# Optimization experiments

Measured on AMD Instinct MI355X. Metric: run time of the kernel, lower is better.

Reference implementation:

```python
import jax, jax.numpy as jnp
import numpy as np

B, S, D = 2, 2048, 1024
E, K, F = 8, 2, 4 * D


def setup_inputs() -> dict:
    key = jax.random.key(0)
    ks = jax.random.split(key, 5)
    sd = 1.0 / np.sqrt(D)
    sf = 1.0 / np.sqrt(F)
    x = jax.random.normal(ks[0], (B, S, D), dtype=jnp.float32)
    Wg = jax.random.uniform(ks[1], (D, E), dtype=jnp.float32, minval=-sd, maxval=sd)
    W1 = jax.random.uniform(ks[2], (E, D, F), dtype=jnp.float32, minval=-sd, maxval=sd)
    W3 = jax.random.uniform(ks[3], (D, E * F), dtype=jnp.float32, minval=-sd, maxval=sd).reshape(D, E, F).transpose(1, 0, 2)
    W2 = jax.random.uniform(ks[4], (E, F, D), dtype=jnp.float32, minval=-sf, maxval=sf)
    return {"x": x, "Wg": Wg, "W1": W1, "W2": W2, "W3": W3}


def reference(x, Wg, W1, W2, W3):
    Bx, Sx, Dx = x.shape
    xf = x.reshape(-1, Dx)  # [T, D]
    T = xf.shape[0]
    gate_logits = xf @ Wg  # [T, E]
    probs = jax.nn.softmax(gate_logits, axis=-1)
    weights, sel = jax.lax.top_k(probs, K)  # [T, K]
    weights = weights / jnp.sum(weights, axis=-1, keepdims=True)
    # scatter top-k weights into a dense [T, E] combine matrix (top-k indices are distinct)
    coef = jnp.zeros((T, W1.shape[0]), dtype=xf.dtype)
    coef = coef.at[jnp.arange(T)[:, None], sel].add(weights)
    out = jnp.zeros_like(xf)
    for e in range(W1.shape[0]):  # small fixed expert count
        h = jax.nn.silu(xf @ W1[e]) * (xf @ W3[e])  # [T, F]
        out = out + coef[:, e:e + 1] * (h @ W2[e])
    aux_loss = jnp.mean(jnp.var(gate_logits, axis=-1, ddof=1))  # torch .var() is unbiased
    return out.reshape(Bx, Sx, Dx), aux_loss
```

## Files before the change

kernel.cpp:

```cpp
#include <hip/hip_runtime.h>

typedef __bf16 bf16x8 __attribute__((ext_vector_type(8)));
typedef float  f32x4  __attribute__((ext_vector_type(4)));

#define TOKS 4096
#define DIM  1024
#define NEXP 8
#define NF   4096
#define CAP  4096
#define BM 128
#define BN 128
#define BK 64

typedef __attribute__((address_space(3))) unsigned int as3_u32;
typedef __attribute__((address_space(1))) unsigned int as1_u32;
__device__ __forceinline__ void gl16(const unsigned short* g, unsigned short* l) {
  __builtin_amdgcn_global_load_lds((as1_u32*)(unsigned long long)g, (as3_u32*)l, 16, 0, 0);
}

__device__ __forceinline__ unsigned short f2bf(float f) {
  unsigned int u = __float_as_uint(f);
  u += 0x7FFFu + ((u >> 16) & 1u);
  return (unsigned short)(u >> 16);
}
__device__ __forceinline__ int swzo(int major) {
  return ((major & 7) ^ ((major >> 3) & 7)) << 3;
}
__device__ __forceinline__ int swz8(int row, int chunk) {
  return (chunk ^ (row & 7)) << 3;
}

__global__ void moe_route(const float* __restrict__ x, const float* __restrict__ Wg,
                          int* __restrict__ pairCnt, int* __restrict__ pairIdx,
                          float* __restrict__ pairWgt, float* __restrict__ auxSum)
{
  int lane = threadIdx.x & 63;
  int tok  = blockIdx.x * 4 + (threadIdx.x >> 6);
  const float* xr = x + (size_t)tok * DIM;
  float acc[8];
  #pragma unroll
  for (int e = 0; e < 8; ++e) acc[e] = 0.f;
  #pragma unroll
  for (int i = 0; i < 16; ++i) {
    int d = i * 64 + lane;
    float xv = xr[d];
    const float4* wr = (const float4*)(Wg + d * 8);
    float4 wa = wr[0], wb = wr[1];
    acc[0] += xv * wa.x; acc[1] += xv * wa.y; acc[2] += xv * wa.z; acc[3] += xv * wa.w;
    acc[4] += xv * wb.x; acc[5] += xv * wb.y; acc[6] += xv * wb.z; acc[7] += xv * wb.w;
  }
  #pragma unroll
  for (int e = 0; e < 8; ++e) {
    float v = acc[e];
    #pragma unroll
    for (int off = 32; off; off >>= 1) v += __shfl_xor(v, off);
    acc[e] = v;
  }
  if (lane == 0) {
    int e1 = 0; float l1 = acc[0];
    #pragma unroll
    for (int e = 1; e < 8; ++e) if (acc[e] > l1) { l1 = acc[e]; e1 = e; }
    int e2 = -1; float l2 = -3.4e38f;
    #pragma unroll
    for (int e = 0; e < 8; ++e) if (e != e1 && acc[e] > l2) { l2 = acc[e]; e2 = e; }
    float r  = expf(l2 - l1);
    float w1 = 1.f / (1.f + r);
    float w2 = r / (1.f + r);
    int s1 = atomicAdd(&pairCnt[e1], 1);
    pairIdx[e1 * CAP + s1] = tok * 2;     pairWgt[e1 * CAP + s1] = w1;
    int s2 = atomicAdd(&pairCnt[e2], 1);
    pairIdx[e2 * CAP + s2] = tok * 2 + 1; pairWgt[e2 * CAP + s2] = w2;
    float m = 0.f;
    #pragma unroll
    for (int e = 0; e < 8; ++e) m += acc[e];
    m *= 0.125f;
    float v = 0.f;
    #pragma unroll
    for (int e = 0; e < 8; ++e) { float dd = acc[e] - m; v += dd * dd; }
    atomicAdd(auxSum, v * (1.f / 7.f));
  }
}

__global__ void moe_aux_final(const float* __restrict__ auxSum, float* __restrict__ outScalar) {
  *outScalar = auxSum[0] * (1.f / (float)TOKS);
}

__global__ __launch_bounds__(256) void cvt_x(const float* __restrict__ in,
                                             unsigned short* __restrict__ o)
{
  int i = (blockIdx.x * 256 + threadIdx.x) * 16;
  const float4* s = (const float4*)(in + i);
  float4 a = s[0], b = s[1], c = s[2], d = s[3];
  union { unsigned short u[8]; uint4 q; } p0, p1;
  p0.u[0]=f2bf(a.x); p0.u[1]=f2bf(a.y); p0.u[2]=f2bf(a.z); p0.u[3]=f2bf(a.w);
  p0.u[4]=f2bf(b.x); p0.u[5]=f2bf(b.y); p0.u[6]=f2bf(b.z); p0.u[7]=f2bf(b.w);
  p1.u[0]=f2bf(c.x); p1.u[1]=f2bf(c.y); p1.u[2]=f2bf(c.z); p1.u[3]=f2bf(c.w);
  p1.u[4]=f2bf(d.x); p1.u[5]=f2bf(d.y); p1.u[6]=f2bf(d.z); p1.u[7]=f2bf(d.w);
  *(uint4*)(o + i)     = p0.q;
  *(uint4*)(o + i + 8) = p1.q;
}

__global__ __launch_bounds__(256) void cvt_transpose(
    const float* __restrict__ in, unsigned short* __restrict__ outp, int R, int C)
{
  __shared__ unsigned short tile[64 * 72];
  int e  = blockIdx.z;
  int r0 = blockIdx.x * 64, c0 = blockIdx.y * 64;
  const float*    ine  = in   + (size_t)e * R * C;
  unsigned short* oute = outp + (size_t)e * R * C;
  int t = threadIdx.x;
  int r = t >> 2, cs = (t & 3) * 16;
  const float4* src = (const float4*)(ine + (size_t)(r0 + r) * C + c0 + cs);
  #pragma unroll
  for (int j = 0; j < 4; ++j) {
    float4 v = src[j];
    tile[(cs + j * 4 + 0) * 72 + r] = f2bf(v.x);
    tile[(cs + j * 4 + 1) * 72 + r] = f2bf(v.y);
    tile[(cs + j * 4 + 2) * 72 + r] = f2bf(v.z);
    tile[(cs + j * 4 + 3) * 72 + r] = f2bf(v.w);
  }
  __syncthreads();
  int c = t >> 2, rs = (t & 3) * 16;
  uint4 o0 = *(const uint4*)&tile[c * 72 + rs];
  uint4 o1 = *(const uint4*)&tile[c * 72 + rs + 8];
  unsigned short* dst = oute + (size_t)(c0 + c) * R + r0 + rs;
  *(uint4*)dst       = o0;
  *(uint4*)(dst + 8) = o1;
}

__global__ __launch_bounds__(256) void cvt_w13(
    const float* __restrict__ W1, const float* __restrict__ W3,
    unsigned short* __restrict__ outp)
{
  __shared__ unsigned short t1[64 * 72];
  __shared__ unsigned short t3[64 * 72];
  int e  = blockIdx.z;
  int r0 = blockIdx.x * 64, c0 = blockIdx.y * 64;
  const float* in1 = W1 + (size_t)e * DIM * NF;
  const float* in3 = W3 + (size_t)e * DIM * NF;
  unsigned short* oute = outp + (size_t)e * (2 * NF) * DIM;
  int t = threadIdx.x;
  int r = t >> 2, cs = (t & 3) * 16;
  const float4* s1 = (const float4*)(in1 + (size_t)(r0 + r) * NF + c0 + cs);
  const float4* s3 = (const float4*)(in3 + (size_t)(r0 + r) * NF + c0 + cs);
  #pragma unroll
  for (int j = 0; j < 4; ++j) {
    float4 v1 = s1[j];
    float4 v3 = s3[j];
    int cb = cs + j * 4;
    t1[(cb + 0) * 72 + r] = f2bf(v1.x);
    t1[(cb + 1) * 72 + r] = f2bf(v1.y);
    t1[(cb + 2) * 72 + r] = f2bf(v1.z);
    t1[(cb + 3) * 72 + r] = f2bf(v1.w);
    t3[(cb + 0) * 72 + r] = f2bf(v3.x);
    t3[(cb + 1) * 72 + r] = f2bf(v3.y);
    t3[(cb + 2) * 72 + r] = f2bf(v3.z);
    t3[(cb + 3) * 72 + r] = f2bf(v3.w);
  }
  __syncthreads();
  int c = t >> 2, rs = (t & 3) * 16;
  int drow = c0 * 2 + (c >> 4) * 32 + (c & 15);
  uint4 a0 = *(const uint4*)&t1[c * 72 + rs];
  uint4 a1 = *(const uint4*)&t1[c * 72 + rs + 8];
  uint4 b0 = *(const uint4*)&t3[c * 72 + rs];
  uint4 b1 = *(const uint4*)&t3[c * 72 + rs + 8];
  unsigned short* d1 = oute + (size_t)drow * DIM + r0 + rs;
  unsigned short* d3 = d1 + (size_t)16 * DIM;
  *(uint4*)d1       = a0;
  *(uint4*)(d1 + 8) = a1;
  *(uint4*)d3       = b0;
  *(uint4*)(d3 + 8) = b1;
}

__global__ __launch_bounds__(512) void moe_ffn1_i(
    const unsigned short* __restrict__ xbf, const unsigned short* __restrict__ W13T,
    const int* __restrict__ pairCnt, const int* __restrict__ pairIdx,
    unsigned short* __restrict__ hbuf)
{
  int bid = blockIdx.x;
  int m_t = (bid >> 3) & 31;
  int n_t = (bid & 7) | (((bid >> 8) & 7) << 3);
  int e   = bid >> 11;
  int cnt = pairCnt[e];
  int m0  = m_t * BM;
  if (m0 >= cnt) return;
  int n0f = n_t * 64;
  __shared__ __attribute__((aligned(16))) unsigned short As[BM * BK];
  __shared__ __attribute__((aligned(16))) unsigned short Bs[BN * BK];
  __shared__ int rowPid[BM];
  int tid = threadIdx.x, lane = tid & 63, wid = tid >> 6;
  if (tid < BM) {
    int gi = m0 + tid;
    rowPid[tid] = (gi < cnt) ? pairIdx[e * CAP + gi] : -1;
  }
  const unsigned short* W13e = W13T + (size_t)e * (2 * NF) * DIM + (size_t)n_t * 128 * DIM;
  f32x4 zero = {0.f, 0.f, 0.f, 0.f};
  f32x4 acc[2][4];
  #pragma unroll
  for (int mi = 0; mi < 2; ++mi)
    #pragma unroll
    for (int ni = 0; ni < 4; ++ni) acc[mi][ni] = zero;
  int wm = (wid >> 1) * 32, wn = (wid & 1) * 64;
  __syncthreads();

  int r0a = wid * 16 + (lane >> 3), r1a = r0a + 8;
  int p0 = rowPid[r0a], p1 = rowPid[r1a];
  size_t tk0 = (size_t)((p0 >= 0) ? (p0 >> 1) : 0);
  size_t tk1 = (size_t)((p1 >= 0) ? (p1 >> 1) : 0);
  int ch0 = ((lane & 7) ^ (r0a & 7)) * 8;
  int ch1 = ((lane & 7) ^ (r1a & 7)) * 8;
  const unsigned short* gA0 = xbf + tk0 * DIM + ch0;
  const unsigned short* gA1 = xbf + tk1 * DIM + ch1;
  const unsigned short* gB0 = W13e + (size_t)r0a * DIM + ch0;
  const unsigned short* gB1 = W13e + (size_t)r1a * DIM + ch1;
  unsigned short* lA0 = &As[(wid * 16) * BK];
  unsigned short* lA1 = &As[(wid * 16 + 8) * BK];
  unsigned short* lB0 = &Bs[(wid * 16) * BK];
  unsigned short* lB1 = &Bs[(wid * 16 + 8) * BK];

  for (int kt = 0; kt < DIM; kt += BK) {
    gl16(gA0 + kt, lA0); gl16(gA1 + kt, lA1);
    gl16(gB0 + kt, lB0); gl16(gB1 + kt, lB1);
    __syncthreads();
    #pragma unroll
    for (int ks = 0; ks < 2; ++ks) {
      int kc = ks * 4 + (lane >> 4);
      bf16x8 af[2];
      #pragma unroll
      for (int mi = 0; mi < 2; ++mi) {
        int row = wm + mi * 16 + (lane & 15);
        af[mi] = *(const bf16x8*)(&As[row * BK + swz8(row, kc)]);
      }
      #pragma unroll
      for (int ni = 0; ni < 4; ++ni) {
        int br = wn + ni * 16 + (lane & 15);
        bf16x8 b = *(const bf16x8*)(&Bs[br * BK + swz8(br, kc)]);
        #pragma unroll
        for (int mi = 0; mi < 2; ++mi)
          acc[mi][ni] = __builtin_amdgcn_mfma_f32_16x16x32_bf16(af[mi], b, acc[mi][ni], 0, 0, 0);
      }
    }
    __syncthreads();
  }
  #pragma unroll
  for (int mi = 0; mi < 2; ++mi) {
    #pragma unroll
    for (int r = 0; r < 4; ++r) {
      int row = wm + mi * 16 + ((lane >> 4) << 2) + r;
      int pid = rowPid[row];
      if (pid < 0) continue;
      size_t hb = (size_t)pid * NF + n0f + (wn >> 1) + (lane & 15);
      #pragma unroll
      for (int fg = 0; fg < 2; ++fg) {
        float a = acc[mi][fg * 2 + 0][r];
        float g = acc[mi][fg * 2 + 1][r];
        float s = 1.f / (1.f + __expf(-a));
        hbuf[hb + fg * 16] = f2bf(a * s * g);
      }
    }
  }
}

__global__ __launch_bounds__(512) void moe_ffn2_g(
    const unsigned short* __restrict__ hbuf, const unsigned short* __restrict__ W2T,
    const int* __restrict__ pairCnt, const int* __restrict__ pairIdx,
    const float* __restrict__ pairWgt, float* __restrict__ out)
{
  int bid = blockIdx.x;
  int n_t = bid & 7;
  int m_t = (bid >> 3) & 31;
  int e   = bid >> 8;
  int cnt = pairCnt[e];
  int m0  = m_t * BM;
  if (m0 >= cnt) return;
  int n0  = n_t * BN;
  __shared__ __attribute__((aligned(16))) unsigned short As[BM * BK];
  __shared__ __attribute__((aligned(16))) unsigned short Bs[BN * BK];
  __shared__ int   rowPid[BM];
  __shared__ float rowW[BM];
  int tid = threadIdx.x, lane = tid & 63, wid = tid >> 6;
  if (tid < BM) {
    int gi = m0 + tid;
    if (gi < cnt) { rowPid[tid] = pairIdx[e * CAP + gi]; rowW[tid] = pairWgt[e * CAP + gi]; }
    else          { rowPid[tid] = -1;                    rowW[tid] = 0.f; }
  }
  const unsigned short* W2e = W2T + (size_t)e * DIM * NF + (size_t)n0 * NF;
  f32x4 zero = {0.f, 0.f, 0.f, 0.f};
  f32x4 acc[2][4];
  #pragma unroll
  for (int mi = 0; mi < 2; ++mi)
    #pragma unroll
    for (int ni = 0; ni < 4; ++ni) acc[mi][ni] = zero;
  int wm = (wid >> 1) * 32, wn = (wid & 1) * 64;
  __syncthreads();

  int r0a = wid * 16 + (lane >> 3), r1a = r0a + 8;
  int p0 = rowPid[r0a], p1 = rowPid[r1a];
  size_t h0 = (size_t)((p0 >= 0) ? p0 : 0);
  size_t h1 = (size_t)((p1 >= 0) ? p1 : 0);
  int ch0 = ((lane & 7) ^ (r0a & 7)) * 8;
  int ch1 = ((lane & 7) ^ (r1a & 7)) * 8;
  const unsigned short* gA0 = hbuf + h0 * NF + ch0;
  const unsigned short* gA1 = hbuf + h1 * NF + ch1;
  const unsigned short* gB0 = W2e + (size_t)r0a * NF + ch0;
  const unsigned short* gB1 = W2e + (size_t)r1a * NF + ch1;
  unsigned short* lA0 = &As[(wid * 16) * BK];
  unsigned short* lA1 = &As[(wid * 16 + 8) * BK];
  unsigned short* lB0 = &Bs[(wid * 16) * BK];
  unsigned short* lB1 = &Bs[(wid * 16 + 8) * BK];

  for (int kt = 0; kt < NF; kt += BK) {
    gl16(gA0 + kt, lA0); gl16(gA1 + kt, lA1);
    gl16(gB0 + kt, lB0); gl16(gB1 + kt, lB1);
    __syncthreads();
    #pragma unroll
    for (int ks = 0; ks < 2; ++ks) {
      int kc = ks * 4 + (lane >> 4);
      bf16x8 af[2];
      #pragma unroll
      for (int mi = 0; mi < 2; ++mi) {
        int row = wm + mi * 16 + (lane & 15);
        af[mi] = *(const bf16x8*)(&As[row * BK + swz8(row, kc)]);
      }
      #pragma unroll
      for (int ni = 0; ni < 4; ++ni) {
        int dc = wn + ni * 16 + (lane & 15);
        bf16x8 b = *(const bf16x8*)(&Bs[dc * BK + swz8(dc, kc)]);
        #pragma unroll
        for (int mi = 0; mi < 2; ++mi)
          acc[mi][ni] = __builtin_amdgcn_mfma_f32_16x16x32_bf16(af[mi], b, acc[mi][ni], 0, 0, 0);
      }
    }
    __syncthreads();
  }
  #pragma unroll
  for (int mi = 0; mi < 2; ++mi) {
    #pragma unroll
    for (int r = 0; r < 4; ++r) {
      int row = wm + mi * 16 + ((lane >> 4) << 2) + r;
      int pid = rowPid[row];
      if (pid < 0) continue;
      float w = rowW[row];
      float* op = out + (size_t)(pid >> 1) * DIM + n0 + wn + (lane & 15);
      #pragma unroll
      for (int ni = 0; ni < 4; ++ni)
        atomicAdd(op + ni * 16, w * acc[mi][ni][r]);
    }
  }
}

__global__ __launch_bounds__(512) void moe_ffn1(
    const float* __restrict__ x, const float* __restrict__ W1, const float* __restrict__ W3,
    const int* __restrict__ pairCnt, const int* __restrict__ pairIdx,
    unsigned short* __restrict__ hbuf)
{
  int e   = blockIdx.z;
  int cnt = pairCnt[e];
  int m0  = blockIdx.x * BM;
  if (m0 >= cnt) return;
  int n0  = blockIdx.y * BN;
  __shared__ __attribute__((aligned(16))) unsigned short As[BM * BK];
  __shared__ __attribute__((aligned(16))) unsigned short B1s[BN * BK];
  __shared__ __attribute__((aligned(16))) unsigned short B3s[BN * BK];
  __shared__ int rowPid[BM];
  int tid = threadIdx.x;
  if (tid < BM) {
    int gi = m0 + tid;
    rowPid[tid] = (gi < cnt) ? pairIdx[e * CAP + gi] : -1;
  }
  const float* W1e = W1 + (size_t)e * DIM * NF;
  const float* W3e = W3 + (size_t)e * DIM * NF;
  f32x4 zero = {0.f, 0.f, 0.f, 0.f};
  f32x4 acc1[2][4], acc2[2][4];
  #pragma unroll
  for (int mi = 0; mi < 2; ++mi)
    #pragma unroll
    for (int ni = 0; ni < 4; ++ni) { acc1[mi][ni] = zero; acc2[mi][ni] = zero; }
  int lane = tid & 63, wid = tid >> 6;
  int wm = (wid >> 1) * 32, wn = (wid & 1) * 64;

  for (int kt = 0; kt < DIM; kt += BK) {
    __syncthreads();
    #pragma unroll
    for (int it = 0; it < 4; ++it) {
      int row = it * 32 + (tid >> 4);
      int dq  = tid & 15;
      int pid = rowPid[row];
      int tk  = (pid >= 0) ? (pid >> 1) : 0;
      float4 v = *(const float4*)(x + (size_t)tk * DIM + kt + dq * 4);
      ushort4 b; b.x = f2bf(v.x); b.y = f2bf(v.y); b.z = f2bf(v.z); b.w = f2bf(v.w);
      *(ushort4*)(&As[row * BK + ((dq * 4) ^ swzo(row))]) = b;
    }
    #pragma unroll
    for (int it = 0; it < 4; ++it) {
      int d  = it * 16 + (tid >> 5);
      int fq = tid & 31;
      size_t go = (size_t)(kt + d) * NF + n0 + fq * 4;
      float4 v1 = *(const float4*)(W1e + go);
      float4 v3 = *(const float4*)(W3e + go);
      const float* p1 = (const float*)&v1;
      const float* p3 = (const float*)&v3;
      #pragma unroll
      for (int i = 0; i < 4; ++i) {
        int f   = fq * 4 + i;
        int idx = f * BK + (d ^ swzo(f));
        B1s[idx] = f2bf(p1[i]);
        B3s[idx] = f2bf(p3[i]);
      }
    }
    __syncthreads();
    #pragma unroll
    for (int ks = 0; ks < 2; ++ks) {
      int kb = ks * 32 + ((lane >> 4) << 3);
      bf16x8 af[2];
      #pragma unroll
      for (int mi = 0; mi < 2; ++mi) {
        int row = wm + mi * 16 + (lane & 15);
        af[mi] = *(const bf16x8*)(&As[row * BK + (kb ^ swzo(row))]);
      }
      #pragma unroll
      for (int ni = 0; ni < 4; ++ni) {
        int f = wn + ni * 16 + (lane & 15);
        bf16x8 b1 = *(const bf16x8*)(&B1s[f * BK + (kb ^ swzo(f))]);
        bf16x8 b3 = *(const bf16x8*)(&B3s[f * BK + (kb ^ swzo(f))]);
        #pragma unroll
        for (int mi = 0; mi < 2; ++mi) {
          acc1[mi][ni] = __builtin_amdgcn_mfma_f32_16x16x32_bf16(af[mi], b1, acc1[mi][ni], 0, 0, 0);
          acc2[mi][ni] = __builtin_amdgcn_mfma_f32_16x16x32_bf16(af[mi], b3, acc2[mi][ni], 0, 0, 0);
        }
      }
    }
  }
  #pragma unroll
  for (int mi = 0; mi < 2; ++mi) {
    #pragma unroll
    for (int r = 0; r < 4; ++r) {
      int row = wm + mi * 16 + ((lane >> 4) << 2) + r;
      int pid = rowPid[row];
      if (pid < 0) continue;
      size_t hb = (size_t)pid * NF + n0 + wn + (lane & 15);
      #pragma unroll
      for (int ni = 0; ni < 4; ++ni) {
        float a = acc1[mi][ni][r];
        float g = acc2[mi][ni][r];
        float s = 1.f / (1.f + __expf(-a));
        hbuf[hb + ni * 16] = f2bf(a * s * g);
      }
    }
  }
}

__global__ __launch_bounds__(512) void moe_ffn2(
    const unsigned short* __restrict__ hbuf, const float* __restrict__ W2,
    const int* __restrict__ pairCnt, const int* __restrict__ pairIdx,
    const float* __restrict__ pairWgt, float* __restrict__ out)
{
  int e   = blockIdx.z;
  int cnt = pairCnt[e];
  int m0  = blockIdx.x * BM;
  if (m0 >= cnt) return;
  int n0  = blockIdx.y * BN;
  __shared__ __attribute__((aligned(16))) unsigned short As[BM * BK];
  __shared__ __attribute__((aligned(16))) unsigned short Bs[BN * BK];
  __shared__ int   rowPid[BM];
  __shared__ float rowW[BM];
  int tid = threadIdx.x;
  if (tid < BM) {
    int gi = m0 + tid;
    if (gi < cnt) { rowPid[tid] = pairIdx[e * CAP + gi]; rowW[tid] = pairWgt[e * CAP + gi]; }
    else          { rowPid[tid] = -1;                    rowW[tid] = 0.f; }
  }
  const float* W2e = W2 + (size_t)e * NF * DIM;
  f32x4 zero = {0.f, 0.f, 0.f, 0.f};
  f32x4 acc[2][4];
  #pragma unroll
  for (int mi = 0; mi < 2; ++mi)
    #pragma unroll
    for (int ni = 0; ni < 4; ++ni) acc[mi][ni] = zero;
  int lane = tid & 63, wid = tid >> 6;
  int wm = (wid >> 1) * 32, wn = (wid & 1) * 64;

  for (int kt = 0; kt < NF; kt += BK) {
    __syncthreads();
    #pragma unroll
    for (int it = 0; it < 2; ++it) {
      int row = it * 64 + (tid >> 3);
      int c8  = tid & 7;
      int pid = rowPid[row];
      int pr  = (pid >= 0) ? pid : 0;
      uint4 v = *(const uint4*)(hbuf + (size_t)pr * NF + kt + c8 * 8);
      *(uint4*)(&As[row * BK + ((c8 * 8) ^ swzo(row))]) = v;
    }
    #pragma unroll
    for (int it = 0; it < 4; ++it) {
      int fk = it * 16 + (tid >> 5);
      int dq = tid & 31;
      float4 v = *(const float4*)(W2e + (size_t)(kt + fk) * DIM + n0 + dq * 4);
      const float* p = (const float*)&v;
      #pragma unroll
      for (int i = 0; i < 4; ++i) {
        int dc = dq * 4 + i;
        Bs[dc * BK + (fk ^ swzo(dc))] = f2bf(p[i]);
      }
    }
    __syncthreads();
    #pragma unroll
    for (int ks = 0; ks < 2; ++ks) {
      int kb = ks * 32 + ((lane >> 4) << 3);
      bf16x8 af[2];
      #pragma unroll
      for (int mi = 0; mi < 2; ++mi) {
        int row = wm + mi * 16 + (lane & 15);
        af[mi] = *(const bf16x8*)(&As[row * BK + (kb ^ swzo(row))]);
      }
      #pragma unroll
      for (int ni = 0; ni < 4; ++ni) {
        int dc = wn + ni * 16 + (lane & 15);
        bf16x8 b = *(const bf16x8*)(&Bs[dc * BK + (kb ^ swzo(dc))]);
        #pragma unroll
        for (int mi = 0; mi < 2; ++mi)
          acc[mi][ni] = __builtin_amdgcn_mfma_f32_16x16x32_bf16(af[mi], b, acc[mi][ni], 0, 0, 0);
      }
    }
  }
  #pragma unroll
  for (int mi = 0; mi < 2; ++mi) {
    #pragma unroll
    for (int r = 0; r < 4; ++r) {
      int row = wm + mi * 16 + ((lane >> 4) << 2) + r;
      int pid = rowPid[row];
      if (pid < 0) continue;
      float w = rowW[row];
      float* op = out + (size_t)(pid >> 1) * DIM + n0 + wn + (lane & 15);
      #pragma unroll
      for (int ni = 0; ni < 4; ++ni)
        atomicAdd(op + ni * 16, w * acc[mi][ni][r]);
    }
  }
}

extern "C" void kernel_launch(void* const* d_in, const int* in_sizes, int n_in,
                              void* d_out, int out_size, void* d_ws, size_t ws_size,
                              hipStream_t stream)
{
  const float* x  = (const float*)d_in[0];
  const float* Wg = (const float*)d_in[1];
  const float* W1 = (const float*)d_in[2];
  const float* W2 = (const float*)d_in[3];
  const float* W3 = (const float*)d_in[4];
  float* out = (float*)d_out;
  char*  ws  = (char*)d_ws;
  int*   pairCnt = (int*)ws;
  float* auxSum  = (float*)(ws + 64);
  int*   pairIdx = (int*)(ws + 4096);
  float* pairWgt = (float*)(ws + 262144);
  unsigned short* xbf  = (unsigned short*)(ws + ((size_t)1 << 20));
  unsigned short* hbuf = (unsigned short*)(ws + ((size_t)9 << 20));
  unsigned short* W13T = (unsigned short*)(ws + ((size_t)73 << 20));
  unsigned short* W2T  = (unsigned short*)(ws + ((size_t)201 << 20));
  const size_t WS_NEED = (size_t)265 << 20;

  hipMemsetAsync(ws, 0, 128, stream);
  hipMemsetAsync(d_out, 0, (size_t)out_size * sizeof(float), stream);
  moe_route<<<TOKS / 4, 256, 0, stream>>>(x, Wg, pairCnt, pairIdx, pairWgt, auxSum);
  moe_aux_final<<<1, 1, 0, stream>>>(auxSum, out + (out_size - 1));

  if (ws_size >= WS_NEED) {
    cvt_x<<<TOKS * DIM / (256 * 16), 256, 0, stream>>>(x, xbf);
    cvt_w13<<<dim3(DIM / 64, NF / 64, NEXP), 256, 0, stream>>>(W1, W3, W13T);
    cvt_transpose<<<dim3(NF / 64, DIM / 64, NEXP), 256, 0, stream>>>(W2, W2T, NF, DIM);
    moe_ffn1_i<<<(TOKS / BM) * (2 * NF / BN) * NEXP, 512, 0, stream>>>(xbf, W13T, pairCnt, pairIdx, hbuf);
    moe_ffn2_g<<<(TOKS / BM) * (DIM / BN) * NEXP, 512, 0, stream>>>(hbuf, W2T, pairCnt, pairIdx, pairWgt, out);
  } else {
    moe_ffn1<<<dim3(TOKS / BM, NF / BN, NEXP), 512, 0, stream>>>(x, W1, W3, pairCnt, pairIdx, hbuf);
    moe_ffn2<<<dim3(TOKS / BM, DIM / BN, NEXP), 512, 0, stream>>>(hbuf, W2, pairCnt, pairIdx, pairWgt, out);
  }
}
```

Baseline: 546.1 us.

## Rewrite FFN1 GEMM as 256x256 double-buffered, phase-interleaved MFMA pipeline

New measurement: 583.3 us. 6.8% more time.

```diff
diff --git a/kernel.cpp b/kernel.cpp
--- a/kernel.cpp
+++ b/kernel.cpp
@@ -172,84 +172,131 @@
   *(uint4*)(d3 + 8) = b1;
 }
 
-__global__ __launch_bounds__(512) void moe_ffn1_i(
+#define FFN1_PHASE(CUR, NXT, KS, Q, STG, DOWAIT, KTN) do {                       \
+  int kc_ = (KS) * 4 + (lane >> 4);                                              \
+  int sz_ = ((kc_ ^ (lane & 7)) << 3);                                           \
+  int ar_ = wr * 128 + (Q) * 64 + (lane & 15);                                   \
+  int br_ = wc * 64 + (lane & 15);                                               \
+  bf16x8 a0_ = *(const bf16x8*)&As_[CUR][(ar_     ) * 64 + sz_];                 \
+  bf16x8 a1_ = *(const bf16x8*)&As_[CUR][(ar_ + 16) * 64 + sz_];                 \
+  bf16x8 a2_ = *(const bf16x8*)&As_[CUR][(ar_ + 32) * 64 + sz_];                 \
+  bf16x8 a3_ = *(const bf16x8*)&As_[CUR][(ar_ + 48) * 64 + sz_];                 \
+  bf16x8 b0_ = *(const bf16x8*)&Bs_[CUR][(br_     ) * 64 + sz_];                 \
+  bf16x8 b1_ = *(const bf16x8*)&Bs_[CUR][(br_ + 16) * 64 + sz_];                 \
+  bf16x8 b2_ = *(const bf16x8*)&Bs_[CUR][(br_ + 32) * 64 + sz_];                 \
+  bf16x8 b3_ = *(const bf16x8*)&Bs_[CUR][(br_ + 48) * 64 + sz_];                 \
+  if ((STG) == 1) {                                                              \
+    gl16(pA[0][0] + (KTN), &As_[NXT][(w * 16      ) * 64]);                      \
+    gl16(pA[0][1] + (KTN), &As_[NXT][(w * 16 +   8) * 64]);                      \
+    gl16(pA[1][0] + (KTN), &As_[NXT][(w * 16 + 128) * 64]);                      \
+    gl16(pA[1][1] + (KTN), &As_[NXT][(w * 16 + 136) * 64]);                      \
+  } else if ((STG) == 2) {                                                       \
+    gl16(pB[0][0] + (KTN), &Bs_[NXT][(w * 16      ) * 64]);                      \
+    gl16(pB[0][1] + (KTN), &Bs_[NXT][(w * 16 +   8) * 64]);                      \
+    gl16(pB[1][0] + (KTN), &Bs_[NXT][(w * 16 + 128) * 64]);                      \
+    gl16(pB[1][1] + (KTN), &Bs_[NXT][(w * 16 + 136) * 64]);                      \
+  }                                                                              \
+  if (DOWAIT) {                                                                  \
+    asm volatile("s_waitcnt lgkmcnt(0)" ::: "memory");                           \
+    asm volatile("s_waitcnt vmcnt(0)" ::: "memory");                             \
+  }                                                                              \
+  __builtin_amdgcn_s_barrier();                                                  \
+  __builtin_amdgcn_s_setprio(1);                                                 \
+  acc[(Q)*4+0][0] = __builtin_amdgcn_mfma_f32_16x16x32_bf16(a0_, b0_, acc[(Q)*4+0][0], 0,0,0); \
+  acc[(Q)*4+1][0] = __builtin_amdgcn_mfma_f32_16x16x32_bf16(a1_, b0_, acc[(Q)*4+1][0], 0,0,0); \
+  acc[(Q)*4+2][0] = __builtin_amdgcn_mfma_f32_16x16x32_bf16(a2_, b0_, acc[(Q)*4+2][0], 0,0,0); \
+  acc[(Q)*4+3][0] = __builtin_amdgcn_mfma_f32_16x16x32_bf16(a3_, b0_, acc[(Q)*4+3][0], 0,0,0); \
+  acc[(Q)*4+0][1] = __builtin_amdgcn_mfma_f32_16x16x32_bf16(a0_, b1_, acc[(Q)*4+0][1], 0,0,0); \
+  acc[(Q)*4+1][1] = __builtin_amdgcn_mfma_f32_16x16x32_bf16(a1_, b1_, acc[(Q)*4+1][1], 0,0,0); \
+  acc[(Q)*4+2][1] = __builtin_amdgcn_mfma_f32_16x16x32_bf16(a2_, b1_, acc[(Q)*4+2][1], 0,0,0); \
+  acc[(Q)*4+3][1] = __builtin_amdgcn_mfma_f32_16x16x32_bf16(a3_, b1_, acc[(Q)*4+3][1], 0,0,0); \
+  acc[(Q)*4+0][2] = __builtin_amdgcn_mfma_f32_16x16x32_bf16(a0_, b2_, acc[(Q)*4+0][2], 0,0,0); \
+  acc[(Q)*4+1][2] = __builtin_amdgcn_mfma_f32_16x16x32_bf16(a1_, b2_, acc[(Q)*4+1][2], 0,0,0); \
+  acc[(Q)*4+2][2] = __builtin_amdgcn_mfma_f32_16x16x32_bf16(a2_, b2_, acc[(Q)*4+2][2], 0,0,0); \
+  acc[(Q)*4+3][2] = __builtin_amdgcn_mfma_f32_16x16x32_bf16(a3_, b2_, acc[(Q)*4+3][2], 0,0,0); \
+  acc[(Q)*4+0][3] = __builtin_amdgcn_mfma_f32_16x16x32_bf16(a0_, b3_, acc[(Q)*4+0][3], 0,0,0); \
+  acc[(Q)*4+1][3] = __builtin_amdgcn_mfma_f32_16x16x32_bf16(a1_, b3_, acc[(Q)*4+1][3], 0,0,0); \
+  acc[(Q)*4+2][3] = __builtin_amdgcn_mfma_f32_16x16x32_bf16(a2_, b3_, acc[(Q)*4+2][3], 0,0,0); \
+  acc[(Q)*4+3][3] = __builtin_amdgcn_mfma_f32_16x16x32_bf16(a3_, b3_, acc[(Q)*4+3][3], 0,0,0); \
+  __builtin_amdgcn_s_setprio(0);                                                 \
+} while (0)
+
+#define FFN1_GROUP(CUR, NXT, KTN)           \
+  FFN1_PHASE(CUR, NXT, 0, 0, 1, 0, KTN);    \
+  FFN1_PHASE(CUR, NXT, 0, 1, 2, 0, KTN);    \
+  FFN1_PHASE(CUR, NXT, 1, 0, 0, 0, KTN);    \
+  FFN1_PHASE(CUR, NXT, 1, 1, 0, 1, KTN);
+
+__global__ __launch_bounds__(512, 2) void moe_ffn1_8p(
     const unsigned short* __restrict__ xbf, const unsigned short* __restrict__ W13T,
     const int* __restrict__ pairCnt, const int* __restrict__ pairIdx,
     unsigned short* __restrict__ hbuf)
 {
   int bid = blockIdx.x;
-  int m_t = (bid >> 3) & 31;
-  int n_t = (bid & 7) | (((bid >> 8) & 7) << 3);
-  int e   = bid >> 11;
+  int n_t = (bid & 7) | (((bid >> 7) & 3) << 3);
+  int m_t = (bid >> 3) & 15;
+  int e   = bid >> 9;
   int cnt = pairCnt[e];
-  int m0  = m_t * BM;
+  int m0  = m_t * 256;
   if (m0 >= cnt) return;
-  int n0f = n_t * 64;
-  __shared__ __attribute__((aligned(16))) unsigned short As[BM * BK];
-  __shared__ __attribute__((aligned(16))) unsigned short Bs[BN * BK];
-  __shared__ int rowPid[BM];
-  int tid = threadIdx.x, lane = tid & 63, wid = tid >> 6;
-  if (tid < BM) {
+  __shared__ __attribute__((aligned(16))) unsigned short As_[2][256 * 64];
+  __shared__ __attribute__((aligned(16))) unsigned short Bs_[2][256 * 64];
+  __shared__ int rowPid[256];
+  int tid = threadIdx.x, lane = tid & 63, w = tid >> 6;
+  if (tid < 256) {
     int gi = m0 + tid;
     rowPid[tid] = (gi < cnt) ? pairIdx[e * CAP + gi] : -1;
   }
-  const unsigned short* W13e = W13T + (size_t)e * (2 * NF) * DIM + (size_t)n_t * 128 * DIM;
+  const unsigned short* W13e = W13T + (size_t)e * (2 * NF) * DIM + (size_t)n_t * 256 * DIM;
+  int wr = w >> 2, wc = w & 3;
   f32x4 zero = {0.f, 0.f, 0.f, 0.f};
-  f32x4 acc[2][4];
-  #pragma unroll
-  for (int mi = 0; mi < 2; ++mi)
+  f32x4 acc[8][4];
+  #pragma unroll
+  for (int mi = 0; mi < 8; ++mi)
     #pragma unroll
     for (int ni = 0; ni < 4; ++ni) acc[mi][ni] = zero;
-  int wm = (wid >> 1) * 32, wn = (wid & 1) * 64;
   __syncthreads();
 
-  int r0a = wid * 16 + (lane >> 3), r1a = r0a + 8;
-  int p0 = rowPid[r0a], p1 = rowPid[r1a];
-  size_t tk0 = (size_t)((p0 >= 0) ? (p0 >> 1) : 0);
-  size_t tk1 = (size_t)((p1 >= 0) ? (p1 >> 1) : 0);
-  int ch0 = ((lane & 7) ^ (r0a & 7)) * 8;
-  int ch1 = ((lane & 7) ^ (r1a & 7)) * 8;
-  const unsigned short* gA0 = xbf + tk0 * DIM + ch0;
-  const unsigned short* gA1 = xbf + tk1 * DIM + ch1;
-  const unsigned short* gB0 = W13e + (size_t)r0a * DIM + ch0;
-  const unsigned short* gB1 = W13e + (size_t)r1a * DIM + ch1;
-  unsigned short* lA0 = &As[(wid * 16) * BK];
-  unsigned short* lA1 = &As[(wid * 16 + 8) * BK];
-  unsigned short* lB0 = &Bs[(wid * 16) * BK];
-  unsigned short* lB1 = &Bs[(wid * 16 + 8) * BK];
-
-  for (int kt = 0; kt < DIM; kt += BK) {
-    gl16(gA0 + kt, lA0); gl16(gA1 + kt, lA1);
-    gl16(gB0 + kt, lB0); gl16(gB1 + kt, lB1);
-    __syncthreads();
-    #pragma unroll
-    for (int ks = 0; ks < 2; ++ks) {
-      int kc = ks * 4 + (lane >> 4);
-      bf16x8 af[2];
-      #pragma unroll
-      for (int mi = 0; mi < 2; ++mi) {
-        int row = wm + mi * 16 + (lane & 15);
-        af[mi] = *(const bf16x8*)(&As[row * BK + swz8(row, kc)]);
-      }
-      #pragma unroll
-      for (int ni = 0; ni < 4; ++ni) {
-        int br = wn + ni * 16 + (lane & 15);
-        bf16x8 b = *(const bf16x8*)(&Bs[br * BK + swz8(br, kc)]);
-        #pragma unroll
-        for (int mi = 0; mi < 2; ++mi)
-          acc[mi][ni] = __builtin_amdgcn_mfma_f32_16x16x32_bf16(af[mi], b, acc[mi][ni], 0, 0, 0);
-      }
-    }
-    __syncthreads();
-  }
-  #pragma unroll
-  for (int mi = 0; mi < 2; ++mi) {
+  int sr = w * 16 + (lane >> 3);
+  int sc = ((lane & 7) ^ (lane >> 3)) * 8;
+  const unsigned short* pA[2][2];
+  const unsigned short* pB[2][2];
+  #pragma unroll
+  for (int h = 0; h < 2; ++h) {
+    #pragma unroll
+    for (int k = 0; k < 2; ++k) {
+      int R = h * 128 + sr + k * 8;
+      int pid = rowPid[R];
+      pA[h][k] = xbf + (size_t)((pid >= 0) ? (pid >> 1) : 0) * DIM + sc;
+      pB[h][k] = W13e + (size_t)R * DIM + sc;
+    }
+  }
+  gl16(pA[0][0], &As_[0][(w * 16      ) * 64]);
+  gl16(pA[0][1], &As_[0][(w * 16 +   8) * 64]);
+  gl16(pA[1][0], &As_[0][(w * 16 + 128) * 64]);
+  gl16(pA[1][1], &As_[0][(w * 16 + 136) * 64]);
+  gl16(pB[0][0], &Bs_[0][(w * 16      ) * 64]);
+  gl16(pB[0][1], &Bs_[0][(w * 16 +   8) * 64]);
+  gl16(pB[1][0], &Bs_[0][(w * 16 + 128) * 64]);
+  gl16(pB[1][1], &Bs_[0][(w * 16 + 136) * 64]);
+  asm volatile("s_waitcnt vmcnt(0)" ::: "memory");
+  __builtin_amdgcn_s_barrier();
+
+  for (int j = 0; j < 16; j += 2) {
+    int ktn0 = (j + 1) * 64;
+    int ktn1 = (j + 2 < 16) ? (j + 2) * 64 : (j + 1) * 64;
+    FFN1_GROUP(0, 1, ktn0);
+    FFN1_GROUP(1, 0, ktn1);
+  }
+
+  #pragma unroll
+  for (int mi = 0; mi < 8; ++mi) {
     #pragma unroll
     for (int r = 0; r < 4; ++r) {
-      int row = wm + mi * 16 + ((lane >> 4) << 2) + r;
+      int row = wr * 128 + mi * 16 + ((lane >> 4) << 2) + r;
       int pid = rowPid[row];
       if (pid < 0) continue;
-      size_t hb = (size_t)pid * NF + n0f + (wn >> 1) + (lane & 15);
+      size_t hb = (size_t)pid * NF + n_t * 128 + wc * 32 + (lane & 15);
       #pragma unroll
       for (int fg = 0; fg < 2; ++fg) {
         float a = acc[mi][fg * 2 + 0][r];
@@ -569,7 +616,7 @@
     cvt_x<<<TOKS * DIM / (256 * 16), 256, 0, stream>>>(x, xbf);
     cvt_w13<<<dim3(DIM / 64, NF / 64, NEXP), 256, 0, stream>>>(W1, W3, W13T);
     cvt_transpose<<<dim3(NF / 64, DIM / 64, NEXP), 256, 0, stream>>>(W2, W2T, NF, DIM);
-    moe_ffn1_i<<<(TOKS / BM) * (2 * NF / BN) * NEXP, 512, 0, stream>>>(xbf, W13T, pairCnt, pairIdx, hbuf);
+    moe_ffn1_8p<<<16 * 32 * NEXP, 512, 0, stream>>>(xbf, W13T, pairCnt, pairIdx, hbuf);
     moe_ffn2_g<<<(TOKS / BM) * (DIM / BN) * NEXP, 512, 0, stream>>>(hbuf, W2T, pairCnt, pairIdx, pairWgt, out);
   } else {
     moe_ffn1<<<dim3(TOKS / BM, NF / BN, NEXP), 512, 0, stream>>>(x, W1, W3, pairCnt, pairIdx, hbuf);
```

## Fuse x bf16 conversion into routing and widen weight transpose tiles

Applied to the files above, without the earlier changes.

Measured after the change: 594.6 us. 1.09x slower.

```diff
diff --git a/kernel.cpp b/kernel.cpp
--- a/kernel.cpp
+++ b/kernel.cpp
@@ -29,10 +29,14 @@
 __device__ __forceinline__ int swz8(int row, int chunk) {
   return (chunk ^ (row & 7)) << 3;
 }
+__device__ __forceinline__ int physk(int k, int f) {
+  return k ^ ((f & 7) << 2) ^ (((f >> 4) & 1) << 5);
+}
 
 __global__ void moe_route(const float* __restrict__ x, const float* __restrict__ Wg,
                           int* __restrict__ pairCnt, int* __restrict__ pairIdx,
-                          float* __restrict__ pairWgt, float* __restrict__ auxSum)
+                          float* __restrict__ pairWgt, float* __restrict__ auxSum,
+                          unsigned short* __restrict__ xbf)
 {
   int lane = threadIdx.x & 63;
   int tok  = blockIdx.x * 4 + (threadIdx.x >> 6);
@@ -44,6 +48,7 @@
   for (int i = 0; i < 16; ++i) {
     int d = i * 64 + lane;
     float xv = xr[d];
+    if (xbf) xbf[(size_t)tok * DIM + d] = f2bf(xv);
     const float4* wr = (const float4*)(Wg + d * 8);
     float4 wa = wr[0], wb = wr[1];
     acc[0] += xv * wa.x; acc[1] += xv * wa.y; acc[2] += xv * wa.z; acc[3] += xv * wa.w;
@@ -85,91 +90,93 @@
   *outScalar = auxSum[0] * (1.f / (float)TOKS);
 }
 
-__global__ __launch_bounds__(256) void cvt_x(const float* __restrict__ in,
-                                             unsigned short* __restrict__ o)
-{
-  int i = (blockIdx.x * 256 + threadIdx.x) * 16;
-  const float4* s = (const float4*)(in + i);
-  float4 a = s[0], b = s[1], c = s[2], d = s[3];
-  union { unsigned short u[8]; uint4 q; } p0, p1;
-  p0.u[0]=f2bf(a.x); p0.u[1]=f2bf(a.y); p0.u[2]=f2bf(a.z); p0.u[3]=f2bf(a.w);
-  p0.u[4]=f2bf(b.x); p0.u[5]=f2bf(b.y); p0.u[6]=f2bf(b.z); p0.u[7]=f2bf(b.w);
-  p1.u[0]=f2bf(c.x); p1.u[1]=f2bf(c.y); p1.u[2]=f2bf(c.z); p1.u[3]=f2bf(c.w);
-  p1.u[4]=f2bf(d.x); p1.u[5]=f2bf(d.y); p1.u[6]=f2bf(d.z); p1.u[7]=f2bf(d.w);
-  *(uint4*)(o + i)     = p0.q;
-  *(uint4*)(o + i + 8) = p1.q;
-}
-
-__global__ __launch_bounds__(256) void cvt_transpose(
-    const float* __restrict__ in, unsigned short* __restrict__ outp, int R, int C)
-{
-  __shared__ unsigned short tile[64 * 72];
-  int e  = blockIdx.z;
-  int r0 = blockIdx.x * 64, c0 = blockIdx.y * 64;
-  const float*    ine  = in   + (size_t)e * R * C;
-  unsigned short* oute = outp + (size_t)e * R * C;
-  int t = threadIdx.x;
-  int r = t >> 2, cs = (t & 3) * 16;
-  const float4* src = (const float4*)(ine + (size_t)(r0 + r) * C + c0 + cs);
-  #pragma unroll
-  for (int j = 0; j < 4; ++j) {
-    float4 v = src[j];
-    tile[(cs + j * 4 + 0) * 72 + r] = f2bf(v.x);
-    tile[(cs + j * 4 + 1) * 72 + r] = f2bf(v.y);
-    tile[(cs + j * 4 + 2) * 72 + r] = f2bf(v.z);
-    tile[(cs + j * 4 + 3) * 72 + r] = f2bf(v.w);
-  }
-  __syncthreads();
-  int c = t >> 2, rs = (t & 3) * 16;
-  uint4 o0 = *(const uint4*)&tile[c * 72 + rs];
-  uint4 o1 = *(const uint4*)&tile[c * 72 + rs + 8];
-  unsigned short* dst = oute + (size_t)(c0 + c) * R + r0 + rs;
-  *(uint4*)dst       = o0;
-  *(uint4*)(dst + 8) = o1;
-}
-
-__global__ __launch_bounds__(256) void cvt_w13(
+__global__ __launch_bounds__(256) void cvt_w13_v2(
     const float* __restrict__ W1, const float* __restrict__ W3,
     unsigned short* __restrict__ outp)
 {
-  __shared__ unsigned short t1[64 * 72];
-  __shared__ unsigned short t3[64 * 72];
+  __shared__ __attribute__((aligned(16))) unsigned int t1[64 * 68];
+  __shared__ __attribute__((aligned(16))) unsigned int t3[64 * 68];
   int e  = blockIdx.z;
-  int r0 = blockIdx.x * 64, c0 = blockIdx.y * 64;
+  int d0 = blockIdx.x * 128, f0 = blockIdx.y * 64;
   const float* in1 = W1 + (size_t)e * DIM * NF;
   const float* in3 = W3 + (size_t)e * DIM * NF;
   unsigned short* oute = outp + (size_t)e * (2 * NF) * DIM;
-  int t = threadIdx.x;
-  int r = t >> 2, cs = (t & 3) * 16;
-  const float4* s1 = (const float4*)(in1 + (size_t)(r0 + r) * NF + c0 + cs);
-  const float4* s3 = (const float4*)(in3 + (size_t)(r0 + r) * NF + c0 + cs);
-  #pragma unroll
-  for (int j = 0; j < 4; ++j) {
-    float4 v1 = s1[j];
-    float4 v3 = s3[j];
-    int cb = cs + j * 4;
-    t1[(cb + 0) * 72 + r] = f2bf(v1.x);
-    t1[(cb + 1) * 72 + r] = f2bf(v1.y);
-    t1[(cb + 2) * 72 + r] = f2bf(v1.z);
-    t1[(cb + 3) * 72 + r] = f2bf(v1.w);
-    t3[(cb + 0) * 72 + r] = f2bf(v3.x);
-    t3[(cb + 1) * 72 + r] = f2bf(v3.y);
-    t3[(cb + 2) * 72 + r] = f2bf(v3.z);
-    t3[(cb + 3) * 72 + r] = f2bf(v3.w);
+  int t   = threadIdx.x;
+  int rr  = (t >> 2) * 2;
+  int cs2 = (t & 3) * 4;
+  int kk  = t >> 2;
+  const float* r1a = in1 + (size_t)(d0 + rr    ) * NF + f0;
+  const float* r1b = in1 + (size_t)(d0 + rr + 1) * NF + f0;
+  const float* r3a = in3 + (size_t)(d0 + rr    ) * NF + f0;
+  const float* r3b = in3 + (size_t)(d0 + rr + 1) * NF + f0;
+  #pragma unroll
+  for (int q = 0; q < 4; ++q) {
+    int fb = cs2 + q * 16;
+    float4 a0 = *(const float4*)(r1a + fb);
+    float4 a1 = *(const float4*)(r1b + fb);
+    float4 b0 = *(const float4*)(r3a + fb);
+    float4 b1 = *(const float4*)(r3b + fb);
+    #pragma unroll
+    for (int i = 0; i < 4; ++i) {
+      int f  = fb + i;
+      int kp = physk(kk, f);
+      t1[f * 68 + kp] = (unsigned)f2bf(((const float*)&a0)[i]) |
+                        ((unsigned)f2bf(((const float*)&a1)[i]) << 16);
+      t3[f * 68 + kp] = (unsigned)f2bf(((const float*)&b0)[i]) |
+                        ((unsigned)f2bf(((const float*)&b1)[i]) << 16);
+    }
   }
   __syncthreads();
-  int c = t >> 2, rs = (t & 3) * 16;
-  int drow = c0 * 2 + (c >> 4) * 32 + (c & 15);
-  uint4 a0 = *(const uint4*)&t1[c * 72 + rs];
-  uint4 a1 = *(const uint4*)&t1[c * 72 + rs + 8];
-  uint4 b0 = *(const uint4*)&t3[c * 72 + rs];
-  uint4 b1 = *(const uint4*)&t3[c * 72 + rs + 8];
-  unsigned short* d1 = oute + (size_t)drow * DIM + r0 + rs;
-  unsigned short* d3 = d1 + (size_t)16 * DIM;
-  *(uint4*)d1       = a0;
-  *(uint4*)(d1 + 8) = a1;
-  *(uint4*)d3       = b0;
-  *(uint4*)(d3 + 8) = b1;
+  int c  = t >> 2;
+  int kb = (t & 3) * 16;
+  int drow = f0 * 2 + ((c >> 4) << 5) + (c & 15);
+  unsigned short* o1 = oute + (size_t)drow * DIM + d0 + kb * 2;
+  unsigned short* o3 = o1 + (size_t)16 * DIM;
+  #pragma unroll
+  for (int i = 0; i < 4; ++i) {
+    int kp = physk(kb + i * 4, c);
+    uint4 v1 = *(const uint4*)&t1[c * 68 + kp];
+    uint4 v3 = *(const uint4*)&t3[c * 68 + kp];
+    *(uint4*)(o1 + i * 8) = v1;
+    *(uint4*)(o3 + i * 8) = v3;
+  }
+}
+
+__global__ __launch_bounds__(256) void cvt_tr_v2(
+    const float* __restrict__ in, unsigned short* __restrict__ outp, int R, int C)
+{
+  __shared__ __attribute__((aligned(16))) unsigned int tl[64 * 68];
+  int e  = blockIdx.z;
+  int r0 = blockIdx.x * 128, c0 = blockIdx.y * 64;
+  const float* ine = in + (size_t)e * R * C;
+  unsigned short* oute = outp + (size_t)e * R * C;
+  int t   = threadIdx.x;
+  int rr  = (t >> 2) * 2;
+  int cs2 = (t & 3) * 4;
+  int kk  = t >> 2;
+  const float* ra = ine + (size_t)(r0 + rr    ) * C + c0;
+  const float* rb = ine + (size_t)(r0 + rr + 1) * C + c0;
+  #pragma unroll
+  for (int q = 0; q < 4; ++q) {
+    int fb = cs2 + q * 16;
+    float4 a0 = *(const float4*)(ra + fb);
+    float4 a1 = *(const float4*)(rb + fb);
+    #pragma unroll
+    for (int i = 0; i < 4; ++i) {
+      int f  = fb + i;
+      tl[f * 68 + physk(kk, f)] = (unsigned)f2bf(((const float*)&a0)[i]) |
+                                  ((unsigned)f2bf(((const float*)&a1)[i]) << 16);
+    }
+  }
+  __syncthreads();
+  int c  = t >> 2;
+  int kb = (t & 3) * 16;
+  unsigned short* o = oute + (size_t)(c0 + c) * R + r0 + kb * 2;
+  #pragma unroll
+  for (int i = 0; i < 4; ++i) {
+    uint4 v = *(const uint4*)&tl[c * 68 + physk(kb + i * 4, c)];
+    *(uint4*)(o + i * 8) = v;
+  }
 }
 
 __global__ __launch_bounds__(512) void moe_ffn1_i(
@@ -559,16 +566,17 @@
   unsigned short* W13T = (unsigned short*)(ws + ((size_t)73 << 20));
   unsigned short* W2T  = (unsigned short*)(ws + ((size_t)201 << 20));
   const size_t WS_NEED = (size_t)265 << 20;
+  bool fast = (ws_size >= WS_NEED);
 
   hipMemsetAsync(ws, 0, 128, stream);
   hipMemsetAsync(d_out, 0, (size_t)out_size * sizeof(float), stream);
-  moe_route<<<TOKS / 4, 256, 0, stream>>>(x, Wg, pairCnt, pairIdx, pairWgt, auxSum);
+  moe_route<<<TOKS / 4, 256, 0, stream>>>(x, Wg, pairCnt, pairIdx, pairWgt, auxSum,
+                                          fast ? xbf : (unsigned short*)nullptr);
   moe_aux_final<<<1, 1, 0, stream>>>(auxSum, out + (out_size - 1));
 
-  if (ws_size >= WS_NEED) {
-    cvt_x<<<TOKS * DIM / (256 * 16), 256, 0, stream>>>(x, xbf);
-    cvt_w13<<<dim3(DIM / 64, NF / 64, NEXP), 256, 0, stream>>>(W1, W3, W13T);
-    cvt_transpose<<<dim3(NF / 64, DIM / 64, NEXP), 256, 0, stream>>>(W2, W2T, NF, DIM);
+  if (fast) {
+    cvt_w13_v2<<<dim3(DIM / 128, NF / 64, NEXP), 256, 0, stream>>>(W1, W3, W13T);
+    cvt_tr_v2<<<dim3(NF / 128, DIM / 64, NEXP), 256, 0, stream>>>(W2, W2T, NF, DIM);
     moe_ffn1_i<<<(TOKS / BM) * (2 * NF / BN) * NEXP, 512, 0, stream>>>(xbf, W13T, pairCnt, pairIdx, hbuf);
     moe_ffn2_g<<<(TOKS / BM) * (DIM / BN) * NEXP, 512, 0, stream>>>(hbuf, W2T, pairCnt, pairIdx, pairWgt, out);
   } else {
```
